# Performance work log

Hardware: AMD Instinct MI355X
Metric: run time of the kernel (lower is better)

Reference implementation:

```python
import jax, jax.numpy as jnp
import numpy as np

N = 50000      # nodes
E = 800000     # edges (avg degree 16)
D_IN = 256
H = 128
D_OUT = 64
L = 3
EPS = 1e-5


def setup_inputs() -> dict:
    key = jax.random.key(0)
    ks = jax.random.split(key, 12)
    s = 0.05
    x = jax.random.normal(ks[0], (N, D_IN), jnp.float32)
    edge_index = jax.random.randint(ks[1], (2, E), 0, N, dtype=jnp.int32)
    edge_attr = jax.random.normal(ks[2], (E,), jnp.float32)
    # in / out projections
    W_in = jax.random.normal(ks[3], (D_IN, H), jnp.float32) * s
    b_in = jnp.zeros((H,), jnp.float32)
    W_out = jax.random.normal(ks[4], (H, D_OUT), jnp.float32) * s
    # per-layer ResGatedGraphConv params (stacked over L layers)
    Wk = jax.random.normal(ks[5], (L, H, H), jnp.float32) * s
    Wq = jax.random.normal(ks[6], (L, H, H), jnp.float32) * s
    Wv = jax.random.normal(ks[7], (L, H, H), jnp.float32) * s
    Ws = jax.random.normal(ks[8], (L, H, H), jnp.float32) * s  # lin_skip (no bias)
    We = jax.random.normal(ks[9], (L, 1, H), jnp.float32) * s  # lin_edge
    bk = jnp.zeros((L, H), jnp.float32)
    bq = jnp.zeros((L, H), jnp.float32)
    bv = jnp.zeros((L, H), jnp.float32)
    be = jnp.zeros((L, H), jnp.float32)
    b_gcn = jnp.zeros((L, H), jnp.float32)  # conv bias
    gamma = jnp.ones((L, H), jnp.float32)
    beta = jnp.zeros((L, H), jnp.float32)
    return {
        "x": x, "edge_attr": edge_attr,
        "W_in": W_in, "b_in": b_in,
        "Wk": Wk, "bk": bk, "Wq": Wq, "bq": bq, "Wv": Wv, "bv": bv,
        "We": We, "be": be, "Ws": Ws, "b_gcn": b_gcn,
        "gamma": gamma, "beta": beta, "W_out": W_out,
        "edge_index": edge_index,
    }


def _layernorm(h, g, b):
    mu = jnp.mean(h, axis=-1, keepdims=True)
    var = jnp.mean((h - mu) ** 2, axis=-1, keepdims=True)
    return (h - mu) * jax.lax.rsqrt(var + EPS) * g + b


def reference(x, edge_attr, W_in, b_in, Wk, bk, Wq, bq, Wv, bv, We, be, Ws,
              b_gcn, gamma, beta, W_out, edge_index):
    src = edge_index[0]  # x_j (source)
    dst = edge_index[1]  # x_i (target)
    ea = edge_attr[:, None]  # [E, 1]
    h = x @ W_in + b_in  # dropout_prob = 0 -> identity
    for l in range(L):
        k = h @ Wk[l] + bk[l]          # lin_key(x_i basis)  [N, H]
        q = h @ Wq[l] + bq[l]          # lin_query(x_j)      [N, H]
        v = h @ Wv[l] + bv[l]          # lin_value(x_j)      [N, H]
        e = ea @ We[l] + be[l]         # lin_edge            [E, H]
        # PyG message: sigmoid((k_i+e) + (q_j+e)) * (v_j+e)
        gate = jax.nn.sigmoid(k[dst] + q[src] + 2.0 * e)
        msg = gate * (v[src] + e)      # [E, H]
        agg = jax.ops.segment_sum(msg, dst, num_segments=N)  # add-aggregation
        h = agg + h @ Ws[l] + b_gcn[l]  # root weight + bias
        h = _layernorm(h, gamma[l], beta[l])
        h = jax.nn.gelu(h, approximate=False)  # torch nn.GELU default (erf)
    return h @ W_out  # out_proj, bias=False
```

## Files before the change

### kernel.cpp

```cpp
#include <hip/hip_runtime.h>

#define N_NODES 50000
#define NPAD    50048
#define E_EDGES 800000
#define DIN 256
#define H 128
#define DOUT 64
#define EPSF 1e-5f
#define NBLK 196
#define RT   1563

typedef __bf16 bf16x8 __attribute__((ext_vector_type(8)));
typedef float  f32x4  __attribute__((ext_vector_type(4)));
typedef unsigned short ushort_t;
typedef unsigned int   uint_t;

#define L2E 1.4426950408889634f
#define LN2 0.6931471805599453f

#if __has_builtin(__builtin_amdgcn_exp2f)
#define EXP2F(x) __builtin_amdgcn_exp2f(x)
#else
#define EXP2F(x) __expf((x) * LN2)
#endif

__device__ inline float bf2f(uint_t u) {
    union { uint_t i; float f; } v; v.i = u << 16; return v.f;
}
__device__ inline ushort_t f2bf(float f) {
    uint_t u = __float_as_uint(f);
    uint_t r = (u + 0x7fffu + ((u >> 16) & 1u)) >> 16;
    return (ushort_t)r;
}

__global__ __launch_bounds__(256) void k_convx(const float* __restrict__ x, ushort_t* __restrict__ xb)
{
    int i = blockIdx.x * 256 + threadIdx.x;
    float4 v = ((const float4*)x)[i];
    ushort4 o;
    o.x = f2bf(v.x); o.y = f2bf(v.y); o.z = f2bf(v.z); o.w = f2bf(v.w);
    ((ushort4*)xb)[i] = o;
}

__global__ __launch_bounds__(256) void k_pack(const float* __restrict__ Wk, const float* __restrict__ Wq,
                                              const float* __restrict__ Wv, const float* __restrict__ Ws,
                                              const float* __restrict__ W_in, const float* __restrict__ W_out,
                                              ushort_t* __restrict__ Bq, ushort_t* __restrict__ Bin,
                                              ushort_t* __restrict__ Bout)
{
    int t = blockIdx.x * 256 + threadIdx.x;
    if (t < 196608) {
        int l = t >> 16;
        int r = t & 65535;
        int c = r >> 7;
        int k = r & 127;
        int m = c >> 7;
        int cm = c & 127;
        const float* W = (m == 0) ? Wk : (m == 1) ? Wq : (m == 2) ? Wv : Ws;
        Bq[t] = f2bf(W[(size_t)l * H * H + k * H + cm]);
    } else if (t < 229376) {
        int t2 = t - 196608;
        int c = t2 >> 8;
        int k = t2 & 255;
        Bin[t2] = f2bf(W_in[k * H + c]);
    } else {
        int t3 = t - 229376;
        int c = t3 >> 7;
        int k = t3 & 127;
        Bout[t3] = f2bf(W_out[k * DOUT + c]);
    }
}

__global__ __launch_bounds__(256) void k_in_mfma(const ushort_t* __restrict__ xb,
                                                 const ushort_t* __restrict__ Bin,
                                                 const float* __restrict__ b_in,
                                                 ushort_t* __restrict__ hb)
{
    int gw = blockIdx.x * 4 + (threadIdx.x >> 6);
    int lane = threadIdx.x & 63;
    int rt = gw >> 2, c32 = (gw & 3) * 32;
    int r0 = rt * 32;
    const ushort_t* Ap = xb + (size_t)(r0 + (lane & 15)) * DIN + 8 * (lane >> 4);
    const ushort_t* Bp = Bin + (size_t)(c32 + (lane & 15)) * DIN + 8 * (lane >> 4);
    f32x4 acc[2][2];
    #pragma unroll
    for (int rb = 0; rb < 2; ++rb)
        #pragma unroll
        for (int nf = 0; nf < 2; ++nf) acc[rb][nf] = (f32x4){0.f, 0.f, 0.f, 0.f};
    #pragma unroll
    for (int ks = 0; ks < 8; ++ks) {
        bf16x8 a0 = *(const bf16x8*)(Ap + ks * 32);
        bf16x8 a1 = *(const bf16x8*)(Ap + 16 * DIN + ks * 32);
        bf16x8 b0 = *(const bf16x8*)(Bp + ks * 32);
        bf16x8 b1 = *(const bf16x8*)(Bp + 16 * DIN + ks * 32);
        acc[0][0] = __builtin_amdgcn_mfma_f32_16x16x32_bf16(a0, b0, acc[0][0], 0, 0, 0);
        acc[1][0] = __builtin_amdgcn_mfma_f32_16x16x32_bf16(a1, b0, acc[1][0], 0, 0, 0);
        acc[0][1] = __builtin_amdgcn_mfma_f32_16x16x32_bf16(a0, b1, acc[0][1], 0, 0, 0);
        acc[1][1] = __builtin_amdgcn_mfma_f32_16x16x32_bf16(a1, b1, acc[1][1], 0, 0, 0);
    }
    int rowoff = (lane >> 4) << 2;
    #pragma unroll
    for (int nf = 0; nf < 2; ++nf) {
        int col = c32 + nf * 16 + (lane & 15);
        float bb = b_in[col];
        #pragma unroll
        for (int rb = 0; rb < 2; ++rb)
            #pragma unroll
            for (int j = 0; j < 4; ++j)
                hb[(size_t)(r0 + rb * 16 + rowoff + j) * H + col] = f2bf(acc[rb][nf][j] + bb);
    }
}

__global__ __launch_bounds__(256) void k_qkvs_mfma(const ushort_t* __restrict__ hb,
                                                   const ushort_t* __restrict__ Bq,
                                                   const float* __restrict__ bk, const float* __restrict__ bq,
                                                   const float* __restrict__ bv, const float* __restrict__ bs,
                                                   ushort_t* __restrict__ ko, uint_t* __restrict__ qv,
                                                   float* __restrict__ agg)
{
    int gw = blockIdx.x * 4 + (threadIdx.x >> 6);
    int lane = threadIdx.x & 63;
    int rt = gw >> 3, cfg = gw & 7;
    int pair = cfg >> 2, c32 = (cfg & 3) * 32;
    int r0 = rt * 32;
    const ushort_t* Ap = hb + (size_t)(r0 + (lane & 15)) * H + 8 * (lane >> 4);
    int cb0 = pair ? 0   : 128;
    int cb1 = pair ? 384 : 256;
    const ushort_t* Bp0 = Bq + (size_t)(cb0 + c32 + (lane & 15)) * H + 8 * (lane >> 4);
    const ushort_t* Bp1 = Bq + (size_t)(cb1 + c32 + (lane & 15)) * H + 8 * (lane >> 4);
    f32x4 acc[2][2][2];
    #pragma unroll
    for (int rb = 0; rb < 2; ++rb)
        #pragma unroll
        for (int m = 0; m < 2; ++m)
            #pragma unroll
            for (int nf = 0; nf < 2; ++nf) acc[rb][m][nf] = (f32x4){0.f, 0.f, 0.f, 0.f};
    #pragma unroll
    for (int ks = 0; ks < 4; ++ks) {
        bf16x8 a0 = *(const bf16x8*)(Ap + ks * 32);
        bf16x8 a1 = *(const bf16x8*)(Ap + 16 * H + ks * 32);
        #pragma unroll
        for (int nf = 0; nf < 2; ++nf) {
            bf16x8 b0 = *(const bf16x8*)(Bp0 + nf * 16 * H + ks * 32);
            bf16x8 b1 = *(const bf16x8*)(Bp1 + nf * 16 * H + ks * 32);
            acc[0][0][nf] = __builtin_amdgcn_mfma_f32_16x16x32_bf16(a0, b0, acc[0][0][nf], 0, 0, 0);
            acc[1][0][nf] = __builtin_amdgcn_mfma_f32_16x16x32_bf16(a1, b0, acc[1][0][nf], 0, 0, 0);
            acc[0][1][nf] = __builtin_amdgcn_mfma_f32_16x16x32_bf16(a0, b1, acc[0][1][nf], 0, 0, 0);
            acc[1][1][nf] = __builtin_amdgcn_mfma_f32_16x16x32_bf16(a1, b1, acc[1][1][nf], 0, 0, 0);
        }
    }
    int rowoff = (lane >> 4) << 2;
    if (pair == 0) {
        #pragma unroll
        for (int nf = 0; nf < 2; ++nf) {
            int col = c32 + nf * 16 + (lane & 15);
            float bbq = bq[col], bbv = bv[col];
            #pragma unroll
            for (int rb = 0; rb < 2; ++rb)
                #pragma unroll
                for (int j = 0; j < 4; ++j) {
                    size_t row = r0 + rb * 16 + rowoff + j;
                    uint_t qb = f2bf((acc[rb][0][nf][j] + bbq) * L2E);
                    uint_t vb = f2bf(acc[rb][1][nf][j] + bbv);
                    qv[row * H + col] = (vb << 16) | qb;
                }
        }
    } else {
        #pragma unroll
        for (int nf = 0; nf < 2; ++nf) {
            int col = c32 + nf * 16 + (lane & 15);
            float bbk = bk[col], bbs = bs[col];
            #pragma unroll
            for (int rb = 0; rb < 2; ++rb)
                #pragma unroll
                for (int j = 0; j < 4; ++j) {
                    size_t row = r0 + rb * 16 + rowoff + j;
                    ko[row * H + col]  = f2bf((acc[rb][0][nf][j] + bbk) * L2E);
                    agg[row * H + col] = acc[rb][1][nf][j] + bbs;
                }
        }
    }
}

__global__ __launch_bounds__(256) void k_hist(const int* __restrict__ ei, int* __restrict__ deg)
{
    int e = blockIdx.x * 256 + threadIdx.x;
    int dst = ei[E_EDGES + e];
    atomicAdd(&deg[dst], 1);
}

__global__ __launch_bounds__(256) void k_bsum(const int* __restrict__ deg, int* __restrict__ bsum)
{
    __shared__ int ws[4];
    int t = threadIdx.x;
    int i = blockIdx.x * 256 + t;
    int v = (i < N_NODES) ? deg[i] : 0;
    #pragma unroll
    for (int off = 32; off > 0; off >>= 1) v += __shfl_down(v, off);
    if ((t & 63) == 0) ws[t >> 6] = v;
    __syncthreads();
    if (t == 0) bsum[blockIdx.x] = ws[0] + ws[1] + ws[2] + ws[3];
}

__global__ __launch_bounds__(256) void k_bscan(const int* __restrict__ bsum, int* __restrict__ boff)
{
    __shared__ int ws[4];
    int t = threadIdx.x;
    int v = (t < NBLK) ? bsum[t] : 0;
    int lane = t & 63, wid = t >> 6;
    int inc = v;
    #pragma unroll
    for (int off = 1; off < 64; off <<= 1) {
        int u = __shfl_up(inc, off);
        if (lane >= off) inc += u;
    }
    if (lane == 63) ws[wid] = inc;
    __syncthreads();
    if (t == 0) {
        int s = 0;
        #pragma unroll
        for (int w = 0; w < 4; ++w) { int x = ws[w]; ws[w] = s; s += x; }
    }
    __syncthreads();
    if (t < NBLK) boff[t] = inc - v + ws[wid];
}

__global__ __launch_bounds__(256) void k_rowptr(const int* __restrict__ deg,
                                                const int* __restrict__ boff,
                                                int* __restrict__ rowptr)
{
    __shared__ int ws[4];
    int t = threadIdx.x;
    int i = blockIdx.x * 256 + t;
    int v = (i < N_NODES) ? deg[i] : 0;
    int lane = t & 63, wid = t >> 6;
    int inc = v;
    #pragma unroll
    for (int off = 1; off < 64; off <<= 1) {
        int u = __shfl_up(inc, off);
        if (lane >= off) inc += u;
    }
    if (lane == 63) ws[wid] = inc;
    __syncthreads();
    if (t == 0) {
        int s = 0;
        #pragma unroll
        for (int w = 0; w < 4; ++w) { int x = ws[w]; ws[w] = s; s += x; }
    }
    __syncthreads();
    int excl = inc - v + ws[wid] + boff[blockIdx.x];
    if (i < N_NODES) rowptr[i] = excl;
    if (i == N_NODES - 1) rowptr[N_NODES] = excl + v;
}

__global__ __launch_bounds__(256) void k_scatter(const int* __restrict__ ei,
                                                 const float* __restrict__ ea,
                                                 const int* __restrict__ rowptr,
                                                 int* __restrict__ fill,
                                                 uint2* __restrict__ csr)
{
    int e = blockIdx.x * 256 + threadIdx.x;
    int src = ei[e];
    int dst = ei[E_EDGES + e];
    int pos = rowptr[dst] + atomicAdd(&fill[dst], 1);
    csr[pos] = make_uint2((uint_t)src, __float_as_uint(ea[e]));
}

__global__ __launch_bounds__(256) void k_agg_ln(const int* __restrict__ rowptr,
                                                const uint2* __restrict__ csr,
                                                const ushort_t* __restrict__ ko,
                                                const uint2* __restrict__ qvp,
                                                const float* __restrict__ aggin,
                                                const float* __restrict__ We,
                                                const float* __restrict__ be,
                                                const float* __restrict__ gamma,
                                                const float* __restrict__ beta,
                                                ushort_t* __restrict__ hout)
{
    int tid = threadIdx.x;
    int lane = tid & 63;
    int node = blockIdx.x * 4 + (tid >> 6);
    int j = lane * 2;

    float2 we  = *(const float2*)(We + j);
    float2 bev = *(const float2*)(be + j);
    float wex = we.x * L2E, wey = we.y * L2E;
    float bex = bev.x * L2E, bey = bev.y * L2E;
    uint_t kdu = ((const uint_t*)ko)[(size_t)node * 64 + lane];
    float kdx = bf2f(kdu & 0xffffu), kdy = bf2f(kdu >> 16);
    float2 acc = ((const float2*)aggin)[(size_t)node * 64 + lane];
    int p = rowptr[node];
    int pend = rowptr[node + 1];

#define GATH(U, A, C) { \
    A = __uint_as_float((C).y); \
    U = qvp[(size_t)(C).x * 64u + lane]; }

#define EDG(U, A) { \
    float qx = __uint_as_float((U).x << 16); \
    float vx = __uint_as_float((U).x & 0xffff0000u); \
    float qy = __uint_as_float((U).y << 16); \
    float vy = __uint_as_float((U).y & 0xffff0000u); \
    float epx = fmaf(A, wex, bex), epy = fmaf(A, wey, bey); \
    float gx = fmaf(2.f, epx, kdx + qx), gy = fmaf(2.f, epy, kdy + qy); \
    float ex2 = EXP2F(-gx), ey2 = EXP2F(-gy); \
    float dx = 1.f + ex2, dy = 1.f + ey2; \
    float r = __builtin_amdgcn_rcpf(dx * dy); \
    float sx = r * dy, sy = r * dx; \
    acc.x = fmaf(sx, fmaf(LN2, epx, vx), acc.x); \
    acc.y = fmaf(sy, fmaf(LN2, epy, vy), acc.y); }

    while (p + 8 <= pend) {
        uint2 c0 = csr[p],     c1 = csr[p + 1], c2 = csr[p + 2], c3 = csr[p + 3];
        uint2 c4 = csr[p + 4], c5 = csr[p + 5], c6 = csr[p + 6], c7 = csr[p + 7];
        uint2 u0, u1, u2, u3, u4, u5, u6, u7;
        float a0, a1, a2, a3, a4, a5, a6, a7;
        GATH(u0, a0, c0); GATH(u1, a1, c1); GATH(u2, a2, c2); GATH(u3, a3, c3);
        GATH(u4, a4, c4); GATH(u5, a5, c5); GATH(u6, a6, c6); GATH(u7, a7, c7);
        EDG(u0, a0); EDG(u1, a1); EDG(u2, a2); EDG(u3, a3);
        EDG(u4, a4); EDG(u5, a5); EDG(u6, a6); EDG(u7, a7);
        p += 8;
    }
    if (p + 4 <= pend) {
        uint2 c0 = csr[p], c1 = csr[p + 1], c2 = csr[p + 2], c3 = csr[p + 3];
        uint2 u0, u1, u2, u3;
        float a0, a1, a2, a3;
        GATH(u0, a0, c0); GATH(u1, a1, c1); GATH(u2, a2, c2); GATH(u3, a3, c3);
        EDG(u0, a0); EDG(u1, a1); EDG(u2, a2); EDG(u3, a3);
        p += 4;
    }
    for (; p < pend; ++p) {
        uint2 c = csr[p];
        uint2 u; float a;
        GATH(u, a, c);
        EDG(u, a);
    }
#undef GATH
#undef EDG

    float s  = acc.x + acc.y;
    float s2 = acc.x * acc.x + acc.y * acc.y;
    #pragma unroll
    for (int off = 32; off > 0; off >>= 1) {
        s  += __shfl_down(s, off);
        s2 += __shfl_down(s2, off);
    }
    s  = __shfl(s, 0);
    s2 = __shfl(s2, 0);
    float mu  = s * (1.f / H);
    float var = s2 * (1.f / H) - mu * mu;
    float rstd = rsqrtf(var + EPSF);
    float2 g = *(const float2*)(gamma + j);
    float2 b = *(const float2*)(beta + j);
    float y0 = (acc.x - mu) * rstd * g.x + b.x;
    float y1 = (acc.y - mu) * rstd * g.y + b.y;
    y0 = 0.5f * y0 * (1.f + erff(y0 * 0.70710678118f));
    y1 = 0.5f * y1 * (1.f + erff(y1 * 0.70710678118f));
    uint_t packed = ((uint_t)f2bf(y1) << 16) | (uint_t)f2bf(y0);
    ((uint_t*)hout)[(size_t)node * 64 + lane] = packed;
}

__global__ __launch_bounds__(256) void k_out_mfma(const ushort_t* __restrict__ hb,
                                                  const ushort_t* __restrict__ Bout,
                                                  float* __restrict__ out)
{
    int gw = blockIdx.x * 4 + (threadIdx.x >> 6);
    if (gw >= 6250) return;
    int lane = threadIdx.x & 63;
    int rg = gw >> 1, cg = gw & 1;
    int r0 = rg * 16, c0 = cg * 32;
    const ushort_t* Ap = hb + (size_t)(r0 + (lane & 15)) * H + 8 * (lane >> 4);
    const ushort_t* Bp = Bout + (size_t)(c0 + (lane & 15)) * H + 8 * (lane >> 4);
    f32x4 acc[2];
    acc[0] = (f32x4){0.f, 0.f, 0.f, 0.f};
    acc[1] = (f32x4){0.f, 0.f, 0.f, 0.f};
    #pragma unroll
    for (int ks = 0; ks < 4; ++ks) {
        bf16x8 a = *(const bf16x8*)(Ap + ks * 32);
        bf16x8 b0 = *(const bf16x8*)(Bp + ks * 32);
        bf16x8 b1 = *(const bf16x8*)(Bp + 16 * H + ks * 32);
        acc[0] = __builtin_amdgcn_mfma_f32_16x16x32_bf16(a, b0, acc[0], 0, 0, 0);
        acc[1] = __builtin_amdgcn_mfma_f32_16x16x32_bf16(a, b1, acc[1], 0, 0, 0);
    }
    int rowb = r0 + ((lane >> 4) << 2);
    #pragma unroll
    for (int nf = 0; nf < 2; ++nf) {
        int col = c0 + nf * 16 + (lane & 15);
        #pragma unroll
        for (int j = 0; j < 4; ++j)
            out[(size_t)(rowb + j) * DOUT + col] = acc[nf][j];
    }
}

extern "C" void kernel_launch(void* const* d_in, const int* in_sizes, int n_in,
                              void* d_out, int out_size, void* d_ws, size_t ws_size,
                              hipStream_t stream) {
    const float* x         = (const float*)d_in[0];
    const float* edge_attr = (const float*)d_in[1];
    const float* W_in      = (const float*)d_in[2];
    const float* b_in      = (const float*)d_in[3];
    const float* Wk        = (const float*)d_in[4];
    const float* bk        = (const float*)d_in[5];
    const float* Wq        = (const float*)d_in[6];
    const float* bq        = (const float*)d_in[7];
    const float* Wv        = (const float*)d_in[8];
    const float* bv        = (const float*)d_in[9];
    const float* We        = (const float*)d_in[10];
    const float* be        = (const float*)d_in[11];
    const float* Ws        = (const float*)d_in[12];
    const float* b_gcn     = (const float*)d_in[13];
    const float* gamma     = (const float*)d_in[14];
    const float* beta      = (const float*)d_in[15];
    const float* W_out     = (const float*)d_in[16];
    const int*   edge_index= (const int*)d_in[17];
    float* out = (float*)d_out;

    char* wsb = (char*)d_ws;
    ushort_t* hb  = (ushort_t*)wsb;                  wsb += (size_t)NPAD * H * 2;
    ushort_t* ko  = (ushort_t*)wsb;                  wsb += (size_t)NPAD * H * 2;
    uint_t*   qv  = (uint_t*)wsb;                    wsb += (size_t)NPAD * H * 4;
    float*    agg = (float*)wsb;                     wsb += (size_t)NPAD * H * 4;
    ushort_t* xb  = (ushort_t*)wsb;                  wsb += (size_t)NPAD * DIN * 2;
    ushort_t* Bq  = (ushort_t*)wsb;                  wsb += 3 * 512 * 128 * 2;
    ushort_t* Bin = (ushort_t*)wsb;                  wsb += 128 * 256 * 2;
    ushort_t* Bout= (ushort_t*)wsb;                  wsb += 64 * 128 * 2;
    uint2* csr    = (uint2*)wsb;                     wsb += (size_t)E_EDGES * 8;
    int*   deg    = (int*)wsb;                       wsb += N_NODES * 4;
    int*   fill   = (int*)wsb;                       wsb += N_NODES * 4;
    int*   rowptr = (int*)wsb;                       wsb += (N_NODES + 1) * 4;
    int*   bsum   = (int*)wsb;                       wsb += NBLK * 4;
    int*   boff   = (int*)wsb;                       wsb += NBLK * 4;

    hipMemsetAsync(deg, 0, 2 * N_NODES * sizeof(int), stream);
    k_hist<<<E_EDGES / 256, 256, 0, stream>>>(edge_index, deg);
    k_bsum<<<NBLK, 256, 0, stream>>>(deg, bsum);
    k_bscan<<<1, 256, 0, stream>>>(bsum, boff);
    k_rowptr<<<NBLK, 256, 0, stream>>>(deg, boff, rowptr);
    k_scatter<<<E_EDGES / 256, 256, 0, stream>>>(edge_index, edge_attr, rowptr, fill, csr);

    k_convx<<<(N_NODES * DIN / 4 + 255) / 256, 256, 0, stream>>>(x, xb);
    k_pack<<<928, 256, 0, stream>>>(Wk, Wq, Wv, Ws, W_in, W_out, Bq, Bin, Bout);

    k_in_mfma<<<RT, 256, 0, stream>>>(xb, Bin, b_in, hb);
    for (int l = 0; l < 3; ++l) {
        k_qkvs_mfma<<<2 * RT, 256, 0, stream>>>(hb, Bq + (size_t)l * 512 * 128,
                                                bk + l * H, bq + l * H, bv + l * H, b_gcn + l * H,
                                                ko, qv, agg);
        k_agg_ln<<<N_NODES / 4, 256, 0, stream>>>(rowptr, csr, ko, (const uint2*)qv, agg,
                                                  We + l * H, be + l * H,
                                                  gamma + l * H, beta + l * H, hb);
    }
    k_out_mfma<<<RT, 256, 0, stream>>>(hb, Bout, out);
}
```

Measured before the change: 456.6 us.

## Store gathered query in FP8 and pack key with skip as bf16

The query projection, which is gathered per edge, is now stored as FP8 (e4m3) in a separate array, and value stays bf16 in its own array. Per-edge gather traffic drops from 8 to 6 bytes per lane. Key and skip output are packed into one bf16 pair buffer, which replaces the fp32 skip accumulator and cuts per-node reads. The feature-to-lane mapping in the aggregation kernel changes to match the packed layout. FP8 queries reduce gate precision and may cost accuracy, and the output stores become 16-bit scattered writes.

```diff
diff --git a/kernel.cpp b/kernel.cpp
--- a/kernel.cpp
+++ b/kernel.cpp
@@ -32,6 +32,41 @@
     uint_t r = (u + 0x7fffu + ((u >> 16) & 1u)) >> 16;
     return (ushort_t)r;
 }
+
+#if __has_builtin(__builtin_amdgcn_cvt_f32_fp8)
+#define FP8DEC(u, s) __builtin_amdgcn_cvt_f32_fp8((uint_t)(u), (s))
+#else
+__device__ inline float fp8_dec_sw(uint_t b) {
+    uint_t s = (b & 0x80u) << 24;
+    uint_t em = b & 0x7fu;
+    if (em < 8u) return __uint_as_float(s);
+    uint_t ex = (em >> 3) + 120u;
+    uint_t mn = (em & 7u) << 20;
+    return __uint_as_float(s | (ex << 23) | mn);
+}
+#define FP8DEC(u, s) fp8_dec_sw(((uint_t)(u) >> (8 * (s))) & 0xffu)
+#endif
+
+#if __has_builtin(__builtin_amdgcn_cvt_pk_fp8_f32)
+__device__ inline uint_t fp8_pk(float a, float b) {
+    return (uint_t)__builtin_amdgcn_cvt_pk_fp8_f32(a, b, 0, false) & 0xffffu;
+}
+#else
+__device__ inline uint_t fp8_enc_sw(float f) {
+    uint_t u = __float_as_uint(f);
+    uint_t s = (u >> 24) & 0x80u;
+    uint_t a = u & 0x7fffffffu;
+    if (a < 0x3c800000u) return s;
+    if (a > 0x43e00000u) a = 0x43e00000u;
+    uint_t r = a + 0x7ffffu + ((a >> 20) & 1u);
+    uint_t ex = (r >> 23) - 120u;
+    uint_t mn = (r >> 20) & 7u;
+    return s | (ex << 3) | mn;
+}
+__device__ inline uint_t fp8_pk(float a, float b) {
+    return fp8_enc_sw(a) | (fp8_enc_sw(b) << 8);
+}
+#endif
 
 __global__ __launch_bounds__(256) void k_convx(const float* __restrict__ x, ushort_t* __restrict__ xb)
 {
@@ -115,8 +150,8 @@
                                                    const ushort_t* __restrict__ Bq,
                                                    const float* __restrict__ bk, const float* __restrict__ bq,
                                                    const float* __restrict__ bv, const float* __restrict__ bs,
-                                                   ushort_t* __restrict__ ko, uint_t* __restrict__ qv,
-                                                   float* __restrict__ agg)
+                                                   ushort_t* __restrict__ qf8, uint_t* __restrict__ vb,
+                                                   uint_t* __restrict__ ks)
 {
     int gw = blockIdx.x * 4 + (threadIdx.x >> 6);
     int lane = threadIdx.x & 63;
@@ -136,13 +171,13 @@
             #pragma unroll
             for (int nf = 0; nf < 2; ++nf) acc[rb][m][nf] = (f32x4){0.f, 0.f, 0.f, 0.f};
     #pragma unroll
-    for (int ks = 0; ks < 4; ++ks) {
-        bf16x8 a0 = *(const bf16x8*)(Ap + ks * 32);
-        bf16x8 a1 = *(const bf16x8*)(Ap + 16 * H + ks * 32);
+    for (int kk = 0; kk < 4; ++kk) {
+        bf16x8 a0 = *(const bf16x8*)(Ap + kk * 32);
+        bf16x8 a1 = *(const bf16x8*)(Ap + 16 * H + kk * 32);
         #pragma unroll
         for (int nf = 0; nf < 2; ++nf) {
-            bf16x8 b0 = *(const bf16x8*)(Bp0 + nf * 16 * H + ks * 32);
-            bf16x8 b1 = *(const bf16x8*)(Bp1 + nf * 16 * H + ks * 32);
+            bf16x8 b0 = *(const bf16x8*)(Bp0 + nf * 16 * H + kk * 32);
+            bf16x8 b1 = *(const bf16x8*)(Bp1 + nf * 16 * H + kk * 32);
             acc[0][0][nf] = __builtin_amdgcn_mfma_f32_16x16x32_bf16(a0, b0, acc[0][0][nf], 0, 0, 0);
             acc[1][0][nf] = __builtin_amdgcn_mfma_f32_16x16x32_bf16(a1, b0, acc[1][0][nf], 0, 0, 0);
             acc[0][1][nf] = __builtin_amdgcn_mfma_f32_16x16x32_bf16(a0, b1, acc[0][1][nf], 0, 0, 0);
@@ -150,33 +185,37 @@
         }
     }
     int rowoff = (lane >> 4) << 2;
+    int l15 = lane & 15;
     if (pair == 0) {
+        int col_lo = c32 + l15, col_hi = col_lo + 16;
+        int e = (c32 >> 1) + l15;
+        float bql = bq[col_lo], bqh = bq[col_hi];
+        float bvl = bv[col_lo], bvh = bv[col_hi];
+        #pragma unroll
+        for (int rb = 0; rb < 2; ++rb)
+            #pragma unroll
+            for (int j = 0; j < 4; ++j) {
+                size_t row = r0 + rb * 16 + rowoff + j;
+                float ql = (acc[rb][0][0][j] + bql) * L2E;
+                float qh = (acc[rb][0][1][j] + bqh) * L2E;
+                qf8[row * 64 + e] = (ushort_t)fp8_pk(ql, qh);
+                uint_t vl = f2bf(acc[rb][1][0][j] + bvl);
+                uint_t vh = f2bf(acc[rb][1][1][j] + bvh);
+                vb[row * 64 + e] = (vh << 16) | vl;
+            }
+    } else {
         #pragma unroll
         for (int nf = 0; nf < 2; ++nf) {
-            int col = c32 + nf * 16 + (lane & 15);
-            float bbq = bq[col], bbv = bv[col];
-            #pragma unroll
-            for (int rb = 0; rb < 2; ++rb)
-                #pragma unroll
-                for (int j = 0; j < 4; ++j) {
-                    size_t row = r0 + rb * 16 + rowoff + j;
-                    uint_t qb = f2bf((acc[rb][0][nf][j] + bbq) * L2E);
-                    uint_t vb = f2bf(acc[rb][1][nf][j] + bbv);
-                    qv[row * H + col] = (vb << 16) | qb;
-                }
-        }
-    } else {
-        #pragma unroll
-        for (int nf = 0; nf < 2; ++nf) {
-            int col = c32 + nf * 16 + (lane & 15);
+            int col = c32 + nf * 16 + l15;
             float bbk = bk[col], bbs = bs[col];
             #pragma unroll
             for (int rb = 0; rb < 2; ++rb)
                 #pragma unroll
                 for (int j = 0; j < 4; ++j) {
                     size_t row = r0 + rb * 16 + rowoff + j;
-                    ko[row * H + col]  = f2bf((acc[rb][0][nf][j] + bbk) * L2E);
-                    agg[row * H + col] = acc[rb][1][nf][j] + bbs;
+                    uint_t kkv = f2bf((acc[rb][0][nf][j] + bbk) * L2E);
+                    uint_t ssv = f2bf(acc[rb][1][nf][j] + bbs);
+                    ks[row * H + col] = (ssv << 16) | kkv;
                 }
         }
     }
@@ -268,9 +307,9 @@
 
 __global__ __launch_bounds__(256) void k_agg_ln(const int* __restrict__ rowptr,
                                                 const uint2* __restrict__ csr,
-                                                const ushort_t* __restrict__ ko,
-                                                const uint2* __restrict__ qvp,
-                                                const float* __restrict__ aggin,
+                                                const ushort_t* __restrict__ qf8,
+                                                const uint_t* __restrict__ vb,
+                                                const uint_t* __restrict__ ks,
                                                 const float* __restrict__ We,
                                                 const float* __restrict__ be,
                                                 const float* __restrict__ gamma,
@@ -280,60 +319,64 @@
     int tid = threadIdx.x;
     int lane = tid & 63;
     int node = blockIdx.x * 4 + (tid >> 6);
-    int j = lane * 2;
-
-    float2 we  = *(const float2*)(We + j);
-    float2 bev = *(const float2*)(be + j);
-    float wex = we.x * L2E, wey = we.y * L2E;
-    float bex = bev.x * L2E, bey = bev.y * L2E;
-    uint_t kdu = ((const uint_t*)ko)[(size_t)node * 64 + lane];
-    float kdx = bf2f(kdu & 0xffffu), kdy = bf2f(kdu >> 16);
-    float2 acc = ((const float2*)aggin)[(size_t)node * 64 + lane];
+    int flo = ((lane >> 4) << 5) + (lane & 15);
+    int fhi = flo + 16;
+
+    float wex = We[flo] * L2E, wey = We[fhi] * L2E;
+    float bex = be[flo] * L2E, bey = be[fhi] * L2E;
+    uint_t klo = ks[(size_t)node * H + flo];
+    uint_t khi = ks[(size_t)node * H + fhi];
+    float kdx = bf2f(klo & 0xffffu), kdy = bf2f(khi & 0xffffu);
+    float2 acc;
+    acc.x = bf2f(klo >> 16);
+    acc.y = bf2f(khi >> 16);
     int p = rowptr[node];
     int pend = rowptr[node + 1];
 
-#define GATH(U, A, C) { \
+#define GATH(QW, UV, A, C) { \
     A = __uint_as_float((C).y); \
-    U = qvp[(size_t)(C).x * 64u + lane]; }
-
-#define EDG(U, A) { \
-    float qx = __uint_as_float((U).x << 16); \
-    float vx = __uint_as_float((U).x & 0xffff0000u); \
-    float qy = __uint_as_float((U).y << 16); \
-    float vy = __uint_as_float((U).y & 0xffff0000u); \
+    QW = (uint_t)qf8[(size_t)(C).x * 64u + lane]; \
+    UV = vb[(size_t)(C).x * 64u + lane]; }
+
+#define EDG(QW, UV, A) { \
+    float qlo = FP8DEC(QW, 0); \
+    float qhi = FP8DEC(QW, 1); \
+    float vlo = __uint_as_float((UV) << 16); \
+    float vhi = __uint_as_float((UV) & 0xffff0000u); \
     float epx = fmaf(A, wex, bex), epy = fmaf(A, wey, bey); \
-    float gx = fmaf(2.f, epx, kdx + qx), gy = fmaf(2.f, epy, kdy + qy); \
+    float gx = fmaf(2.f, epx, kdx + qlo), gy = fmaf(2.f, epy, kdy + qhi); \
     float ex2 = EXP2F(-gx), ey2 = EXP2F(-gy); \
     float dx = 1.f + ex2, dy = 1.f + ey2; \
     float r = __builtin_amdgcn_rcpf(dx * dy); \
-    float sx = r * dy, sy = r * dx; \
-    acc.x = fmaf(sx, fmaf(LN2, epx, vx), acc.x); \
-    acc.y = fmaf(sy, fmaf(LN2, epy, vy), acc.y); }
+    acc.x = fmaf(r * dy, fmaf(LN2, epx, vlo), acc.x); \
+    acc.y = fmaf(r * dx, fmaf(LN2, epy, vhi), acc.y); }
 
     while (p + 8 <= pend) {
         uint2 c0 = csr[p],     c1 = csr[p + 1], c2 = csr[p + 2], c3 = csr[p + 3];
         uint2 c4 = csr[p + 4], c5 = csr[p + 5], c6 = csr[p + 6], c7 = csr[p + 7];
-        uint2 u0, u1, u2, u3, u4, u5, u6, u7;
+        uint_t q0, q1, q2, q3, q4, q5, q6, q7;
+        uint_t u0, u1, u2, u3, u4, u5, u6, u7;
         float a0, a1, a2, a3, a4, a5, a6, a7;
-        GATH(u0, a0, c0); GATH(u1, a1, c1); GATH(u2, a2, c2); GATH(u3, a3, c3);
-        GATH(u4, a4, c4); GATH(u5, a5, c5); GATH(u6, a6, c6); GATH(u7, a7, c7);
-        EDG(u0, a0); EDG(u1, a1); EDG(u2, a2); EDG(u3, a3);
-        EDG(u4, a4); EDG(u5, a5); EDG(u6, a6); EDG(u7, a7);
+        GATH(q0, u0, a0, c0); GATH(q1, u1, a1, c1); GATH(q2, u2, a2, c2); GATH(q3, u3, a3, c3);
+        GATH(q4, u4, a4, c4); GATH(q5, u5, a5, c5); GATH(q6, u6, a6, c6); GATH(q7, u7, a7, c7);
+        EDG(q0, u0, a0); EDG(q1, u1, a1); EDG(q2, u2, a2); EDG(q3, u3, a3);
+        EDG(q4, u4, a4); EDG(q5, u5, a5); EDG(q6, u6, a6); EDG(q7, u7, a7);
         p += 8;
     }
     if (p + 4 <= pend) {
         uint2 c0 = csr[p], c1 = csr[p + 1], c2 = csr[p + 2], c3 = csr[p + 3];
-        uint2 u0, u1, u2, u3;
+        uint_t q0, q1, q2, q3;
+        uint_t u0, u1, u2, u3;
         float a0, a1, a2, a3;
-        GATH(u0, a0, c0); GATH(u1, a1, c1); GATH(u2, a2, c2); GATH(u3, a3, c3);
-        EDG(u0, a0); EDG(u1, a1); EDG(u2, a2); EDG(u3, a3);
+        GATH(q0, u0, a0, c0); GATH(q1, u1, a1, c1); GATH(q2, u2, a2, c2); GATH(q3, u3, a3, c3);
+        EDG(q0, u0, a0); EDG(q1, u1, a1); EDG(q2, u2, a2); EDG(q3, u3, a3);
         p += 4;
     }
     for (; p < pend; ++p) {
         uint2 c = csr[p];
-        uint2 u; float a;
-        GATH(u, a, c);
-        EDG(u, a);
+        uint_t qw, uv; float a;
+        GATH(qw, uv, a, c);
+        EDG(qw, uv, a);
     }
 #undef GATH
 #undef EDG
@@ -350,14 +393,14 @@
     float mu  = s * (1.f / H);
     float var = s2 * (1.f / H) - mu * mu;
     float rstd = rsqrtf(var + EPSF);
-    float2 g = *(const float2*)(gamma + j);
-    float2 b = *(const float2*)(beta + j);
-    float y0 = (acc.x - mu) * rstd * g.x + b.x;
-    float y1 = (acc.y - mu) * rstd * g.y + b.y;
+    float glo = gamma[flo], ghi = gamma[fhi];
+    float blo = beta[flo],  bhi = beta[fhi];
+    float y0 = (acc.x - mu) * rstd * glo + blo;
+    float y1 = (acc.y - mu) * rstd * ghi + bhi;
     y0 = 0.5f * y0 * (1.f + erff(y0 * 0.70710678118f));
     y1 = 0.5f * y1 * (1.f + erff(y1 * 0.70710678118f));
-    uint_t packed = ((uint_t)f2bf(y1) << 16) | (uint_t)f2bf(y0);
-    ((uint_t*)hout)[(size_t)node * 64 + lane] = packed;
+    hout[(size_t)node * H + flo] = f2bf(y0);
+    hout[(size_t)node * H + fhi] = f2bf(y1);
 }
 
 __global__ __launch_bounds__(256) void k_out_mfma(const ushort_t* __restrict__ hb,
@@ -375,10 +418,10 @@
     acc[0] = (f32x4){0.f, 0.f, 0.f, 0.f};
     acc[1] = (f32x4){0.f, 0.f, 0.f, 0.f};
     #pragma unroll
-    for (int ks = 0; ks < 4; ++ks) {
-        bf16x8 a = *(const bf16x8*)(Ap + ks * 32);
-        bf16x8 b0 = *(const bf16x8*)(Bp + ks * 32);
-        bf16x8 b1 = *(const bf16x8*)(Bp + 16 * H + ks * 32);
+    for (int kk = 0; kk < 4; ++kk) {
+        bf16x8 a = *(const bf16x8*)(Ap + kk * 32);
+        bf16x8 b0 = *(const bf16x8*)(Bp + kk * 32);
+        bf16x8 b1 = *(const bf16x8*)(Bp + 16 * H + kk * 32);
         acc[0] = __builtin_amdgcn_mfma_f32_16x16x32_bf16(a, b0, acc[0], 0, 0, 0);
         acc[1] = __builtin_amdgcn_mfma_f32_16x16x32_bf16(a, b1, acc[1], 0, 0, 0);
     }
@@ -417,9 +460,9 @@
 
     char* wsb = (char*)d_ws;
     ushort_t* hb  = (ushort_t*)wsb;                  wsb += (size_t)NPAD * H * 2;
-    ushort_t* ko  = (ushort_t*)wsb;                  wsb += (size_t)NPAD * H * 2;
-    uint_t*   qv  = (uint_t*)wsb;                    wsb += (size_t)NPAD * H * 4;
-    float*    agg = (float*)wsb;                     wsb += (size_t)NPAD * H * 4;
+    ushort_t* qf8 = (ushort_t*)wsb;                  wsb += (size_t)NPAD * 64 * 2;
+    uint_t*   vb  = (uint_t*)wsb;                    wsb += (size_t)NPAD * 64 * 4;
+    uint_t*   ks  = (uint_t*)wsb;                    wsb += (size_t)NPAD * H * 4;
     ushort_t* xb  = (ushort_t*)wsb;                  wsb += (size_t)NPAD * DIN * 2;
     ushort_t* Bq  = (ushort_t*)wsb;                  wsb += 3 * 512 * 128 * 2;
     ushort_t* Bin = (ushort_t*)wsb;                  wsb += 128 * 256 * 2;
@@ -445,8 +488,8 @@
     for (int l = 0; l < 3; ++l) {
         k_qkvs_mfma<<<2 * RT, 256, 0, stream>>>(hb, Bq + (size_t)l * 512 * 128,
                                                 bk + l * H, bq + l * H, bv + l * H, b_gcn + l * H,
-                                                ko, qv, agg);
-        k_agg_ln<<<N_NODES / 4, 256, 0, stream>>>(rowptr, csr, ko, (const uint2*)qv, agg,
+                                                qf8, vb, ks);
+        k_agg_ln<<<N_NODES / 4, 256, 0, stream>>>(rowptr, csr, qf8, vb, ks,
                                                   We + l * H, be + l * H,
                                                   gamma + l * H, beta + l * H, hb);
     }
```

Result: faster. 424.7 us (-7.0%).
